# Optimization experiments

Hardware: AMD Instinct MI355X
Metric: run time of the kernel (lower is better)

The kernel has to match this reference:

```python
import jax, jax.numpy as jnp
import numpy as np

TOPK = 21
N_ITEMS = 100000
EMBED_DIM = 128
BATCH = 4096
HIST_LEN = 50


def setup_inputs() -> dict:
    key = jax.random.key(0)
    k1, k2, k3 = jax.random.split(key, 3)
    emb = jax.random.normal(k1, (N_ITEMS, EMBED_DIM), dtype=jnp.float32) * 0.02
    item_seq = jax.random.randint(k2, (BATCH, HIST_LEN), 0, N_ITEMS, dtype=jnp.int32)
    item_seq_len = jax.random.randint(k3, (BATCH,), 1, HIST_LEN + 1, dtype=jnp.int32)
    return {"item_seq": item_seq, "item_seq_len": item_seq_len, "emb": emb}


def reference(item_seq, item_seq_len, emb):
    # --- recommender_model.forward: masked mean-pool session encoder -> query [B, D]
    seq_emb = emb[item_seq]                                   # [B, L, D] gather
    L = item_seq.shape[1]
    mask = (jnp.arange(L)[None, :] < item_seq_len[:, None])   # [B, L]
    denom = jnp.maximum(item_seq_len, 1).astype(emb.dtype)[:, None]
    query = (seq_emb * mask[..., None].astype(emb.dtype)).sum(axis=1) / denom  # [B, D]

    # --- mm+topk path: dense scores against full item table, then top-k
    scores = jnp.einsum('bd,vd->bv', query, emb)              # [B, V] (HBM round-trip)
    values, indices = jax.lax.top_k(scores, TOPK)             # [B, topk]
    return values, indices
```

## Files before the change

kernel.cpp:

```cpp
#include <hip/hip_runtime.h>
#include <stdint.h>

#define V_ITEMS 100000
#define EDIM    128
#define BATCH   4096
#define HLEN    50
#define TOPK    21

#define MT      64
#define MS      4
#define VSPLIT  4
#define NCHUNK_TOT (V_ITEMS / 16)
#define NCH_MAX ((NCHUNK_TOT + VSPLIT - 1) / VSPLIT)
#define NITER   ((NCH_MAX + 7) / 8)
#define CAP2    256
#define NKEEP   32
#define NCAND   (NKEEP * VSPLIT)

typedef __attribute__((ext_vector_type(8))) short          bf16x8;
typedef __attribute__((ext_vector_type(4))) float          f32x4;
typedef __attribute__((ext_vector_type(8))) unsigned short u16x8;

__device__ inline unsigned short f2bf(float x) {
    unsigned u = __float_as_uint(x);
    return (unsigned short)((u + 0x7FFFu + ((u >> 16) & 1u)) >> 16);
}

__global__ __launch_bounds__(256) void conv_bf16(
        const float* __restrict__ s, unsigned short* __restrict__ d) {
    size_t i = (size_t)blockIdx.x * 256 + threadIdx.x;
    const float4* sp = (const float4*)s + i * 2;
    float4 a = sp[0], b = sp[1];
    u16x8 o;
    o[0] = f2bf(a.x); o[1] = f2bf(a.y); o[2] = f2bf(a.z); o[3] = f2bf(a.w);
    o[4] = f2bf(b.x); o[5] = f2bf(b.y); o[6] = f2bf(b.z); o[7] = f2bf(b.w);
    *((u16x8*)d + i) = o;
}

__global__ __launch_bounds__(EDIM) void query_bf16(
        const int* __restrict__ seq, const int* __restrict__ len,
        const float* __restrict__ emb, unsigned short* __restrict__ qbf) {
    int b = blockIdx.x, d = threadIdx.x;
    int n = len[b];
    float s = 0.f;
    for (int l = 0; l < n; l++)
        s += emb[(size_t)seq[b * HLEN + l] * EDIM + d];
    qbf[b * EDIM + d] = f2bf(s / (float)(n > 0 ? n : 1));
}

__device__ inline void compact_batch(float* cv, int* ci, int* cnt, float* thr,
                                     int b, int lane) {
    int n = min(cnt[b], CAP2);
    float val[4]; int idx[4]; unsigned key[4];
    #pragma unroll
    for (int e = 0; e < 4; e++) {
        int i = lane + e * 64;
        if (i < n) {
            float v = cv[b * CAP2 + i];
            unsigned u = __float_as_uint(v);
            key[e] = (u & 0x80000000u) ? ~u : (u | 0x80000000u);
            val[e] = v; idx[e] = ci[b * CAP2 + i];
        } else { key[e] = 0u; val[e] = 0.f; idx[e] = 0; }
    }
    unsigned cur = 0u;
    #pragma unroll 1
    for (int bit = 31; bit >= 0; bit--) {
        unsigned mid = cur | (1u << bit);
        int c = 0;
        #pragma unroll
        for (int e = 0; e < 4; e++)
            c += __popcll(__ballot(key[e] >= mid));
        if (c >= 32) cur = mid;
    }
    int base = 0;
    #pragma unroll
    for (int e = 0; e < 4; e++) {
        bool keep = key[e] >= cur;
        unsigned long long m = __ballot(keep);
        int p = base + (int)__popcll(m & ((1ull << lane) - 1ull));
        if (keep && p < NKEEP) { cv[b * CAP2 + p] = val[e]; ci[b * CAP2 + p] = idx[e]; }
        base += (int)__popcll(m);
    }
    if (lane == 0) {
        cnt[b] = NKEEP;
        thr[b] = (cur & 0x80000000u) ? __uint_as_float(cur ^ 0x80000000u)
                                     : __uint_as_float(~cur);
    }
}

__global__ __launch_bounds__(512, 2) void score_topk(
        const unsigned short* __restrict__ qbf,
        const unsigned short* __restrict__ ebf,
        int* __restrict__ candOut) {
    __shared__ float cv[MT * CAP2];
    __shared__ int   ci[MT * CAP2];
    __shared__ int   cnt[MT];
    __shared__ float thr[MT];

    const int tid  = threadIdx.x;
    const int lane = tid & 63;
    const int w    = tid >> 6;
    const int r    = blockIdx.x & (VSPLIT - 1);
    const int mg   = blockIdx.x / VSPLIT;
    const int b0   = mg * MT;
    const int n15  = lane & 15, quad = lane >> 4;

    const int cstart = (r * NCHUNK_TOT) / VSPLIT;
    const int nch    = ((r + 1) * NCHUNK_TOT) / VSPLIT - cstart;

    if (tid < MT) { cnt[tid] = 0; thr[tid] = -INFINITY; }
    __syncthreads();

    bf16x8 afr[MS][4];
    #pragma unroll
    for (int ms = 0; ms < MS; ms++)
        #pragma unroll
        for (int t = 0; t < 4; t++)
            afr[ms][t] = *(const bf16x8*)(qbf + (b0 + ms * 16 + n15) * EDIM
                                          + t * 32 + quad * 8);
    float thrR[MS * 4];
    #pragma unroll
    for (int i = 0; i < MS * 4; i++) thrR[i] = -INFINITY;

    const unsigned short* bbase = ebf + ((size_t)cstart * 16 + n15) * EDIM + quad * 8;

    int nextEvt = 1;

    auto body = [&](int iter, bf16x8 (&cur)[4], bf16x8 (&nxt)[4]) {
        {
            int nit   = (iter + 1 < NITER) ? (iter + 1) : iter;
            int pch   = nit * 8 + w;
            int pcc   = (pch < nch) ? pch : (nch - 1);
            const unsigned short* bp = bbase + (size_t)pcc * (16 * EDIM);
            #pragma unroll
            for (int t = 0; t < 4; t++) nxt[t] = *(const bf16x8*)(bp + t * 32);
        }
        f32x4 acc[MS];
        #pragma unroll
        for (int ms = 0; ms < MS; ms++) acc[ms] = (f32x4){0.f, 0.f, 0.f, 0.f};
        #pragma unroll
        for (int t = 0; t < 4; t++)
            #pragma unroll
            for (int ms = 0; ms < MS; ms++)
                acc[ms] = __builtin_amdgcn_mfma_f32_16x16x32_bf16(afr[ms][t], cur[t], acc[ms], 0, 0, 0);

        int chunk = iter * 8 + w;
        bool act  = chunk < nch;
        if (act) {
            int item = (cstart + chunk) * 16 + n15;
            float s[MS * 4]; bool hit = false;
            #pragma unroll
            for (int k = 0; k < MS * 4; k++) {
                float v = acc[k >> 2][k & 3];
                s[k] = v;
                hit |= (v > thrR[k]);
            }
            if (__any(hit)) {
                #pragma unroll
                for (int k = 0; k < MS * 4; k++) {
                    if (s[k] > thrR[k]) {
                        int row = (k >> 2) * 16 + (quad << 2) + (k & 3);
                        int pz = atomicAdd(&cnt[row], 1);
                        if (pz < CAP2) { cv[row * CAP2 + pz] = s[k]; ci[row * CAP2 + pz] = item; }
                    }
                }
            }
        }
        if (iter + 1 == nextEvt || iter + 1 == NITER) {
            if (iter + 1 == nextEvt) nextEvt <<= 1;
            bool fin = (iter + 1 == NITER);
            __syncthreads();
            #pragma unroll 1
            for (int j = 0; j < 8; j++) {
                int b = (w << 3) + j;
                if (fin || cnt[b] > 96) compact_batch(cv, ci, cnt, thr, b, lane);
            }
            __syncthreads();
            #pragma unroll
            for (int ms = 0; ms < MS; ms++)
                #pragma unroll
                for (int rr = 0; rr < 4; rr++)
                    thrR[ms * 4 + rr] = thr[ms * 16 + (quad << 2) + rr];
        }
    };

    bf16x8 bA[4], bB[4];
    {
        int cc0 = (w < nch) ? w : (nch - 1);
        const unsigned short* bp = bbase + (size_t)cc0 * (16 * EDIM);
        #pragma unroll
        for (int t = 0; t < 4; t++) bA[t] = *(const bf16x8*)(bp + t * 32);
    }
    for (int iter = 0; iter < NITER; iter += 2) {
        body(iter,     bA, bB);
        body(iter + 1, bB, bA);
    }

    for (int j = 0; j < 8; j++) {
        int b = (w << 3) + j;
        if (lane < NKEEP)
            candOut[(b0 + b) * NCAND + r * NKEEP + lane] = ci[b * CAP2 + lane];
    }
}

__global__ __launch_bounds__(256) void rescore(
        const int* __restrict__ seq, const int* __restrict__ len,
        const float* __restrict__ emb, const int* __restrict__ cand,
        float* __restrict__ out) {
    __shared__ double qd[EDIM];
    __shared__ double sv[NCAND];
    __shared__ int    si[NCAND];
    int b = blockIdx.x, t = threadIdx.x;
    int n = len[b];
    if (t < EDIM) {
        double s = 0.0;
        for (int l = 0; l < n; l++)
            s += (double)emb[(size_t)seq[b * HLEN + l] * EDIM + t];
        qd[t] = s / (double)(n > 0 ? n : 1);
    }
    __syncthreads();

    int c = t >> 1, h = t & 1;
    int idx = cand[b * NCAND + c];
    const float4* ev = (const float4*)(emb + (size_t)idx * EDIM + h * 64);
    double part = 0.0;
    #pragma unroll 4
    for (int j = 0; j < 16; j++) {
        float4 e = ev[j];
        int d = h * 64 + j * 4;
        part += qd[d] * (double)e.x + qd[d + 1] * (double)e.y
              + qd[d + 2] * (double)e.z + qd[d + 3] * (double)e.w;
    }
    part += __shfl_xor(part, 1);
    if (h == 0) { sv[c] = part; si[c] = idx; }
    __syncthreads();

    if (t < NCAND) {
        double v = sv[t]; int id = si[t];
        int rank = 0;
        for (int j = 0; j < NCAND; j++) {
            double vj = sv[j]; int ij = si[j];
            rank += (vj > v || (vj == v && ij < id)) ? 1 : 0;
        }
        if (rank < TOPK) {
            out[(size_t)b * TOPK + rank] = (float)v;
            out[(size_t)BATCH * TOPK + (size_t)b * TOPK + rank] = (float)id;
        }
    }
}

extern "C" void kernel_launch(void* const* d_in, const int* in_sizes, int n_in,
                              void* d_out, int out_size, void* d_ws, size_t ws_size,
                              hipStream_t stream) {
    const int*   seq = (const int*)d_in[0];
    const int*   len = (const int*)d_in[1];
    const float* emb = (const float*)d_in[2];
    float* out = (float*)d_out;

    unsigned short* qbf  = (unsigned short*)d_ws;
    unsigned short* ebf  = qbf + (size_t)BATCH * EDIM;
    int*            cand = (int*)(ebf + (size_t)V_ITEMS * EDIM);

    conv_bf16 <<<(V_ITEMS * EDIM) / (256 * 8), 256, 0, stream>>>(emb, ebf);
    query_bf16<<<BATCH, EDIM, 0, stream>>>(seq, len, emb, qbf);
    score_topk<<<(BATCH / MT) * VSPLIT, 512, 0, stream>>>(qbf, ebf, cand);
    rescore   <<<BATCH, 256, 0, stream>>>(seq, len, emb, cand, out);
}
```

Measured before the change: 516.7 us.

## Replace LDS atomic candidate append with per-wave ballot-compacted segments

Candidate collection in the score/top-k kernel no longer uses shared-memory atomicAdd per passing score. Each wave now writes into its own fixed 32-slot segment per row, using ballot and popcount to find positions, and values and indices are packed together as uint2. Compaction runs at every event point over the kept 32 entries plus 8 wave segments. This removes LDS atomic contention and divergent branches. In exchange every score does an unconditional LDS store (to a dump slot when it fails), and a segment that fills up between compactions silently drops candidates, which could hurt accuracy early on when the threshold is low.

After: 623.3 us. 1.21x slower.

```diff
diff --git a/kernel.cpp b/kernel.cpp
--- a/kernel.cpp
+++ b/kernel.cpp
@@ -13,8 +13,9 @@
 #define NCHUNK_TOT (V_ITEMS / 16)
 #define NCH_MAX ((NCHUNK_TOT + VSPLIT - 1) / VSPLIT)
 #define NITER   ((NCH_MAX + 7) / 8)
-#define CAP2    256
 #define NKEEP   32
+#define SEGSZ   32
+#define CAPR    (NKEEP + 8 * SEGSZ)
 #define NCAND   (NKEEP * VSPLIT)
 
 typedef __attribute__((ext_vector_type(8))) short          bf16x8;
@@ -48,19 +49,24 @@
     qbf[b * EDIM + d] = f2bf(s / (float)(n > 0 ? n : 1));
 }
 
-__device__ inline void compact_batch(float* cv, int* ci, int* cnt, float* thr,
-                                     int b, int lane) {
-    int n = min(cnt[b], CAP2);
-    float val[4]; int idx[4]; unsigned key[4];
-    #pragma unroll
-    for (int e = 0; e < 4; e++) {
+__device__ inline void compact_row(uint2* cb, const int* segcnt, int* ncomp,
+                                   float* thr, int b, int lane) {
+    int nc = ncomp[b];
+    unsigned key[5]; unsigned vraw[5]; unsigned item[5];
+    #pragma unroll
+    for (int e = 0; e < 5; e++) {
         int i = lane + e * 64;
-        if (i < n) {
-            float v = cv[b * CAP2 + i];
-            unsigned u = __float_as_uint(v);
+        bool v;
+        if (i < NKEEP)      v = (i < nc);
+        else if (i < CAPR)  v = ((i - NKEEP) & (SEGSZ - 1)) <
+                                segcnt[b * 8 + ((i - NKEEP) >> 5)];
+        else                v = false;
+        if (v) {
+            uint2 d = cb[b * CAPR + i];
+            unsigned u = d.x;
             key[e] = (u & 0x80000000u) ? ~u : (u | 0x80000000u);
-            val[e] = v; idx[e] = ci[b * CAP2 + i];
-        } else { key[e] = 0u; val[e] = 0.f; idx[e] = 0; }
+            vraw[e] = u; item[e] = d.y;
+        } else { key[e] = 0u; vraw[e] = 0u; item[e] = 0u; }
     }
     unsigned cur = 0u;
     #pragma unroll 1
@@ -68,21 +74,22 @@
         unsigned mid = cur | (1u << bit);
         int c = 0;
         #pragma unroll
-        for (int e = 0; e < 4; e++)
+        for (int e = 0; e < 5; e++)
             c += __popcll(__ballot(key[e] >= mid));
-        if (c >= 32) cur = mid;
+        if (c >= NKEEP) cur = mid;
     }
     int base = 0;
     #pragma unroll
-    for (int e = 0; e < 4; e++) {
+    for (int e = 0; e < 5; e++) {
         bool keep = key[e] >= cur;
-        unsigned long long m = __ballot(keep);
-        int p = base + (int)__popcll(m & ((1ull << lane) - 1ull));
-        if (keep && p < NKEEP) { cv[b * CAP2 + p] = val[e]; ci[b * CAP2 + p] = idx[e]; }
-        base += (int)__popcll(m);
+        unsigned long long mm = __ballot(keep);
+        int p = base + (int)__popcll(mm & ((1ull << lane) - 1ull));
+        if (keep && p < NKEEP)
+            cb[b * CAPR + p] = make_uint2(vraw[e], item[e]);
+        base += (int)__popcll(mm);
     }
     if (lane == 0) {
-        cnt[b] = NKEEP;
+        ncomp[b] = NKEEP;
         thr[b] = (cur & 0x80000000u) ? __uint_as_float(cur ^ 0x80000000u)
                                      : __uint_as_float(~cur);
     }
@@ -92,9 +99,9 @@
         const unsigned short* __restrict__ qbf,
         const unsigned short* __restrict__ ebf,
         int* __restrict__ candOut) {
-    __shared__ float cv[MT * CAP2];
-    __shared__ int   ci[MT * CAP2];
-    __shared__ int   cnt[MT];
+    __shared__ uint2 cb[MT * CAPR + 64];
+    __shared__ int   segcnt[MT * 8];
+    __shared__ int   ncomp[MT];
     __shared__ float thr[MT];
 
     const int tid  = threadIdx.x;
@@ -104,11 +111,13 @@
     const int mg   = blockIdx.x / VSPLIT;
     const int b0   = mg * MT;
     const int n15  = lane & 15, quad = lane >> 4;
+    const unsigned lm15 = (1u << n15) - 1u;
+    const int dumpslot = MT * CAPR + lane;
 
     const int cstart = (r * NCHUNK_TOT) / VSPLIT;
     const int nch    = ((r + 1) * NCHUNK_TOT) / VSPLIT - cstart;
 
-    if (tid < MT) { cnt[tid] = 0; thr[tid] = -INFINITY; }
+    if (tid < MT) { ncomp[tid] = 0; thr[tid] = -INFINITY; }
     __syncthreads();
 
     bf16x8 afr[MS][4];
@@ -118,9 +127,16 @@
         for (int t = 0; t < 4; t++)
             afr[ms][t] = *(const bf16x8*)(qbf + (b0 + ms * 16 + n15) * EDIM
                                           + t * 32 + quad * 8);
-    float thrR[MS * 4];
-    #pragma unroll
-    for (int i = 0; i < MS * 4; i++) thrR[i] = -INFINITY;
+    float thrR[16];
+    int   curk[16];
+    int   rowbase[16];
+    #pragma unroll
+    for (int k = 0; k < 16; k++) {
+        thrR[k] = -INFINITY;
+        curk[k] = 0;
+        rowbase[k] = ((k >> 2) * 16 + (quad << 2) + (k & 3)) * CAPR
+                     + NKEEP + w * SEGSZ;
+    }
 
     const unsigned short* bbase = ebf + ((size_t)cstart * 16 + n15) * EDIM + quad * 8;
 
@@ -147,40 +163,40 @@
         int chunk = iter * 8 + w;
         bool act  = chunk < nch;
         if (act) {
-            int item = (cstart + chunk) * 16 + n15;
-            float s[MS * 4]; bool hit = false;
-            #pragma unroll
-            for (int k = 0; k < MS * 4; k++) {
-                float v = acc[k >> 2][k & 3];
-                s[k] = v;
-                hit |= (v > thrR[k]);
+            unsigned item = (unsigned)((cstart + chunk) * 16 + n15);
+            #pragma unroll
+            for (int k = 0; k < 16; k++) {
+                float sv = acc[k >> 2][k & 3];
+                bool pass = sv > thrR[k];
+                unsigned long long m = __ballot(pass);
+                unsigned qm = (unsigned)((m >> (quad << 4)) & 0xFFFFull);
+                int pos  = curk[k] + __popc(qm & lm15);
+                int cnew = curk[k] + __popc(qm);
+                curk[k] = cnew > SEGSZ ? SEGSZ : cnew;
+                bool ok = pass && (pos < SEGSZ);
+                int slot = ok ? (rowbase[k] + pos) : dumpslot;
+                cb[slot] = make_uint2(__float_as_uint(sv), item);
             }
-            if (__any(hit)) {
+        }
+        if (iter + 1 == nextEvt || iter + 1 == NITER) {
+            if (iter + 1 == nextEvt) nextEvt <<= 1;
+            if (n15 == 0) {
                 #pragma unroll
-                for (int k = 0; k < MS * 4; k++) {
-                    if (s[k] > thrR[k]) {
-                        int row = (k >> 2) * 16 + (quad << 2) + (k & 3);
-                        int pz = atomicAdd(&cnt[row], 1);
-                        if (pz < CAP2) { cv[row * CAP2 + pz] = s[k]; ci[row * CAP2 + pz] = item; }
-                    }
+                for (int k = 0; k < 16; k++) {
+                    int row = (k >> 2) * 16 + (quad << 2) + (k & 3);
+                    segcnt[row * 8 + w] = curk[k];
                 }
             }
-        }
-        if (iter + 1 == nextEvt || iter + 1 == NITER) {
-            if (iter + 1 == nextEvt) nextEvt <<= 1;
-            bool fin = (iter + 1 == NITER);
             __syncthreads();
             #pragma unroll 1
-            for (int j = 0; j < 8; j++) {
-                int b = (w << 3) + j;
-                if (fin || cnt[b] > 96) compact_batch(cv, ci, cnt, thr, b, lane);
+            for (int j = 0; j < 8; j++)
+                compact_row(cb, segcnt, ncomp, thr, (w << 3) + j, lane);
+            __syncthreads();
+            #pragma unroll
+            for (int k = 0; k < 16; k++) {
+                curk[k] = 0;
+                thrR[k] = thr[(k >> 2) * 16 + (quad << 2) + (k & 3)];
             }
-            __syncthreads();
-            #pragma unroll
-            for (int ms = 0; ms < MS; ms++)
-                #pragma unroll
-                for (int rr = 0; rr < 4; rr++)
-                    thrR[ms * 4 + rr] = thr[ms * 16 + (quad << 2) + rr];
         }
     };
 
@@ -199,7 +215,8 @@
     for (int j = 0; j < 8; j++) {
         int b = (w << 3) + j;
         if (lane < NKEEP)
-            candOut[(b0 + b) * NCAND + r * NKEEP + lane] = ci[b * CAP2 + lane];
+            candOut[(b0 + b) * NCAND + r * NKEEP + lane] =
+                (int)cb[b * CAPR + lane].y;
     }
 }
 
```

## Double vocabulary split and waves per block; reuse fp32 query in rescore

Applied to the files above, without the earlier changes.

The scoring kernel splits the item table 8 ways instead of 4 and runs 16 waves per 1024-thread block, with a fixed iteration count and a tighter register bound from launch_bounds. The goal is more concurrent waves and blocks to hide memory latency during the streamed MFMA scoring. The query kernel now also writes an fp32 query, so rescore no longer repeats the per-row gather and double-precision mean. In exchange, rescore must handle twice as many candidates per row. The 128-VGPR cap implied by four waves per SIMD may cause register spills in the scoring loop.

After: 778.8 us. +50.7%, slower.

```diff
diff --git a/kernel.cpp b/kernel.cpp
--- a/kernel.cpp
+++ b/kernel.cpp
@@ -9,10 +9,10 @@
 
 #define MT      64
 #define MS      4
-#define VSPLIT  4
+#define VSPLIT  8
+#define NWAVE   16
 #define NCHUNK_TOT (V_ITEMS / 16)
-#define NCH_MAX ((NCHUNK_TOT + VSPLIT - 1) / VSPLIT)
-#define NITER   ((NCH_MAX + 7) / 8)
+#define NITER   50
 #define CAP2    256
 #define NKEEP   32
 #define NCAND   (NKEEP * VSPLIT)
@@ -39,13 +39,16 @@
 
 __global__ __launch_bounds__(EDIM) void query_bf16(
         const int* __restrict__ seq, const int* __restrict__ len,
-        const float* __restrict__ emb, unsigned short* __restrict__ qbf) {
+        const float* __restrict__ emb, unsigned short* __restrict__ qbf,
+        float* __restrict__ qf) {
     int b = blockIdx.x, d = threadIdx.x;
     int n = len[b];
     float s = 0.f;
     for (int l = 0; l < n; l++)
         s += emb[(size_t)seq[b * HLEN + l] * EDIM + d];
-    qbf[b * EDIM + d] = f2bf(s / (float)(n > 0 ? n : 1));
+    float q = s / (float)(n > 0 ? n : 1);
+    qbf[b * EDIM + d] = f2bf(q);
+    qf [b * EDIM + d] = q;
 }
 
 __device__ inline void compact_batch(float* cv, int* ci, int* cnt, float* thr,
@@ -70,7 +73,7 @@
         #pragma unroll
         for (int e = 0; e < 4; e++)
             c += __popcll(__ballot(key[e] >= mid));
-        if (c >= 32) cur = mid;
+        if (c >= NKEEP) cur = mid;
     }
     int base = 0;
     #pragma unroll
@@ -88,7 +91,7 @@
     }
 }
 
-__global__ __launch_bounds__(512, 2) void score_topk(
+__global__ __launch_bounds__(1024, 4) void score_topk(
         const unsigned short* __restrict__ qbf,
         const unsigned short* __restrict__ ebf,
         int* __restrict__ candOut) {
@@ -129,7 +132,7 @@
     auto body = [&](int iter, bf16x8 (&cur)[4], bf16x8 (&nxt)[4]) {
         {
             int nit   = (iter + 1 < NITER) ? (iter + 1) : iter;
-            int pch   = nit * 8 + w;
+            int pch   = nit * NWAVE + w;
             int pcc   = (pch < nch) ? pch : (nch - 1);
             const unsigned short* bp = bbase + (size_t)pcc * (16 * EDIM);
             #pragma unroll
@@ -144,7 +147,7 @@
             for (int ms = 0; ms < MS; ms++)
                 acc[ms] = __builtin_amdgcn_mfma_f32_16x16x32_bf16(afr[ms][t], cur[t], acc[ms], 0, 0, 0);
 
-        int chunk = iter * 8 + w;
+        int chunk = iter * NWAVE + w;
         bool act  = chunk < nch;
         if (act) {
             int item = (cstart + chunk) * 16 + n15;
@@ -171,8 +174,8 @@
             bool fin = (iter + 1 == NITER);
             __syncthreads();
             #pragma unroll 1
-            for (int j = 0; j < 8; j++) {
-                int b = (w << 3) + j;
+            for (int j = 0; j < MT / NWAVE; j++) {
+                int b = w * (MT / NWAVE) + j;
                 if (fin || cnt[b] > 96) compact_batch(cv, ci, cnt, thr, b, lane);
             }
             __syncthreads();
@@ -196,28 +199,21 @@
         body(iter + 1, bB, bA);
     }
 
-    for (int j = 0; j < 8; j++) {
-        int b = (w << 3) + j;
+    for (int j = 0; j < MT / NWAVE; j++) {
+        int b = w * (MT / NWAVE) + j;
         if (lane < NKEEP)
             candOut[(b0 + b) * NCAND + r * NKEEP + lane] = ci[b * CAP2 + lane];
     }
 }
 
-__global__ __launch_bounds__(256) void rescore(
-        const int* __restrict__ seq, const int* __restrict__ len,
-        const float* __restrict__ emb, const int* __restrict__ cand,
-        float* __restrict__ out) {
+__global__ __launch_bounds__(512) void rescore(
+        const float* __restrict__ qf, const float* __restrict__ emb,
+        const int* __restrict__ cand, float* __restrict__ out) {
     __shared__ double qd[EDIM];
     __shared__ double sv[NCAND];
     __shared__ int    si[NCAND];
     int b = blockIdx.x, t = threadIdx.x;
-    int n = len[b];
-    if (t < EDIM) {
-        double s = 0.0;
-        for (int l = 0; l < n; l++)
-            s += (double)emb[(size_t)seq[b * HLEN + l] * EDIM + t];
-        qd[t] = s / (double)(n > 0 ? n : 1);
-    }
+    if (t < EDIM) qd[t] = (double)qf[b * EDIM + t];
     __syncthreads();
 
     int c = t >> 1, h = t & 1;
@@ -260,9 +256,10 @@
     unsigned short* qbf  = (unsigned short*)d_ws;
     unsigned short* ebf  = qbf + (size_t)BATCH * EDIM;
     int*            cand = (int*)(ebf + (size_t)V_ITEMS * EDIM);
+    float*          qf   = (float*)(cand + (size_t)BATCH * NCAND);
 
     conv_bf16 <<<(V_ITEMS * EDIM) / (256 * 8), 256, 0, stream>>>(emb, ebf);
-    query_bf16<<<BATCH, EDIM, 0, stream>>>(seq, len, emb, qbf);
-    score_topk<<<(BATCH / MT) * VSPLIT, 512, 0, stream>>>(qbf, ebf, cand);
-    rescore   <<<BATCH, 256, 0, stream>>>(seq, len, emb, cand, out);
-}
+    query_bf16<<<BATCH, EDIM, 0, stream>>>(seq, len, emb, qbf, qf);
+    score_topk<<<(BATCH / MT) * VSPLIT, 1024, 0, stream>>>(qbf, ebf, cand);
+    rescore   <<<BATCH, 512, 0, stream>>>(qf, emb, cand, out);
+}
```
